# Performance work log

Hardware: AMD Instinct MI355X
Metric: run time of the kernel (lower is better)

## Reference

```python
import jax, jax.numpy as jnp
import numpy as np

N_SAMPLE = 32
RADIUS = 0.25
NORMALIZE_DP = True

B, N, K, C = 8, 8192, 2048, 64


def setup_inputs() -> dict:
    key = jax.random.key(0)
    k1, k2, k3 = jax.random.split(key, 3)
    points = jax.random.uniform(k1, (B, N, 3), dtype=jnp.float32)
    centroids = jax.random.uniform(k2, (B, K, 3), dtype=jnp.float32)
    features = jax.random.normal(k3, (B, C, N), dtype=jnp.float32)
    return {"points": points, "centroids": centroids, "features": features}


def _ball_query(points, centroids, n_sample, radius):
    # points: (B,N,3), centroids: (B,K,3) -> indices (B,K,n_sample) int32
    # squared distances via |c|^2 + |p|^2 - 2 c.p to avoid a (B,K,N,3) temp
    cp = jnp.einsum("bkd,bnd->bkn", centroids, points)  # (B,K,N)
    d2 = (
        jnp.sum(centroids * centroids, -1)[:, :, None]
        + jnp.sum(points * points, -1)[:, None, :]
        - 2.0 * cp
    )
    mask = d2 < radius * radius  # (B,K,N)
    # stable argsort on ~mask puts in-ball indices first, in ascending order
    order = jnp.argsort(jnp.logical_not(mask), axis=-1, stable=True)
    idx = order[..., :n_sample]  # (B,K,S)
    count = jnp.sum(mask, axis=-1, keepdims=True)  # (B,K,1)
    slot = jnp.arange(n_sample)[None, None, :]
    # CUDA ball_query semantics: pad empty slots with the first found index
    idx = jnp.where(slot < count, idx, idx[..., :1])
    return idx


def reference(points, centroids, features):
    idx = _ball_query(points, centroids, N_SAMPLE, RADIUS)  # (B,K,S)
    # gather points: (B,K,S,3)
    gp = jax.vmap(lambda p, i: p[i])(points, idx)
    gp = gp - centroids[:, :, None, :]  # centroid subtract
    if NORMALIZE_DP:
        gp = gp / RADIUS
    grouped_pts = jnp.transpose(gp, (0, 3, 1, 2))  # (B,3,K,S)
    # gather features: (B,C,K,S)
    new_feats = jax.vmap(lambda f, i: f[:, i])(features, idx)
    return grouped_pts, new_feats
```

## Files before the change

### kernel.cpp

```cpp
#include <hip/hip_runtime.h>

constexpr int B = 8;
constexpr int N = 8192;
constexpr int K = 2048;
constexpr int C = 64;
constexpr int NS = 32;
#define RAD2 0.0625f

__global__ __launch_bounds__(256) void ballquery_gp_kernel(
    const float* __restrict__ points,
    const float* __restrict__ centroids,
    float* __restrict__ gp_out,
    int* __restrict__ idx_ws)
{
#pragma clang fp contract(off)
    const int wave = (blockIdx.x * blockDim.x + threadIdx.x) >> 6;
    const int lane = threadIdx.x & 63;
    if (wave >= B * K) return;
    const int b = wave / K;
    const int k = wave - b * K;

    const float* cptr = centroids + (size_t)(b * K + k) * 3;
    const float c0 = cptr[0], c1 = cptr[1], c2 = cptr[2];
    const float cc = (c0 * c0 + c1 * c1) + c2 * c2;

    const float* pbase = points + (size_t)b * N * 3;
    int* idxrow = idx_ws + (size_t)wave * NS;
    float* gpb = gp_out + ((size_t)b * 3 * K + k) * NS;

    int count = 0;
    int idx0 = 0;

    for (int base = 0; base < N; base += 64) {
        const int i = base + lane;
        const float p0 = pbase[i * 3 + 0];
        const float p1 = pbase[i * 3 + 1];
        const float p2 = pbase[i * 3 + 2];
        const float pp = (p0 * p0 + p1 * p1) + p2 * p2;
        const float cp = (c0 * p0 + c1 * p1) + c2 * p2;
        const float d2 = (cc + pp) - 2.0f * cp;
        const bool hit = d2 < RAD2;
        const unsigned long long m = __ballot(hit);
        if (hit) {
            const unsigned long long below = m & ((1ull << lane) - 1ull);
            const int pos = count + __popcll(below);
            if (pos < NS) {
                idxrow[pos] = i;
                gpb[0 * K * NS + pos] = (p0 - c0) * 4.0f;
                gpb[1 * K * NS + pos] = (p1 - c1) * 4.0f;
                gpb[2 * K * NS + pos] = (p2 - c2) * 4.0f;
            }
        }
        if (count == 0 && m != 0ull) idx0 = base + __builtin_ctzll(m);
        count += __popcll(m);
        if (count >= NS) break;
    }

    const int cnt = count < NS ? count : NS;
    if (lane >= cnt && lane < NS) {
        const float p0 = pbase[idx0 * 3 + 0];
        const float p1 = pbase[idx0 * 3 + 1];
        const float p2 = pbase[idx0 * 3 + 2];
        idxrow[lane] = idx0;
        gpb[0 * K * NS + lane] = (p0 - c0) * 4.0f;
        gpb[1 * K * NS + lane] = (p1 - c1) * 4.0f;
        gpb[2 * K * NS + lane] = (p2 - c2) * 4.0f;
    }
}

__global__ __launch_bounds__(1024) void gather_feats_lds(
    const float* __restrict__ features,
    const int* __restrict__ idx_ws,
    float* __restrict__ nf_out)
{
    __shared__ float row[N];
    const int bc = blockIdx.x;
    const int t = threadIdx.x;

    {
        const float4* frow4 = reinterpret_cast<const float4*>(features + (size_t)bc * N);
        float4* row4 = reinterpret_cast<float4*>(row);
#pragma unroll
        for (int j = 0; j < 2; ++j)
            row4[t + j * 1024] = frow4[t + j * 1024];
    }
    __syncthreads();

    const int b = bc >> 6;
    const int* idxb = idx_ws + (size_t)b * K * NS;
    float* outb = nf_out + (size_t)bc * K * NS;

#pragma unroll
    for (int j = 0; j < 16; ++j) {
        const int g = j * 1024 + t;
        const int4 iv = *reinterpret_cast<const int4*>(idxb + (size_t)g * 4);
        float4 v;
        v.x = row[iv.x];
        v.y = row[iv.y];
        v.z = row[iv.z];
        v.w = row[iv.w];
        *reinterpret_cast<float4*>(outb + (size_t)g * 4) = v;
    }
}

extern "C" void kernel_launch(void* const* d_in, const int* in_sizes, int n_in,
                              void* d_out, int out_size, void* d_ws, size_t ws_size,
                              hipStream_t stream) {
    const float* points    = (const float*)d_in[0];
    const float* centroids = (const float*)d_in[1];
    const float* features  = (const float*)d_in[2];
    float* out = (float*)d_out;

    float* gp_out = out;
    float* nf_out = out + (size_t)B * 3 * K * NS;
    int* idx_ws = (int*)d_ws;

    const int waves = B * K;
    const int blocksA = waves / 4;
    hipLaunchKernelGGL(ballquery_gp_kernel, dim3(blocksA), dim3(256), 0, stream,
                       points, centroids, gp_out, idx_ws);

    hipLaunchKernelGGL(gather_feats_lds, dim3(B * C), dim3(1024), 0, stream,
                       features, idx_ws, nf_out);
}
```

Before: 61.06 us.

## Prefetch next point chunk, use nontemporal gather I/O, shrink ball-query blocks

In the ball-query kernel, the next 64-point chunk is software-prefetched into registers while the current chunk is tested, so load latency is hidden behind the distance computation. The block size drops from 256 to 128 threads and the div/mod is replaced with shifts. In the feature gather, index loads are double-buffered, and the feature-row loads and output stores use nontemporal builtins to reduce cache pollution. The prefetch adds one redundant chunk load per wave on early exit, and the nontemporal hints may interact unpredictably with L2 reuse.

```diff
diff --git a/kernel.cpp b/kernel.cpp
--- a/kernel.cpp
+++ b/kernel.cpp
@@ -7,7 +7,10 @@
 constexpr int NS = 32;
 #define RAD2 0.0625f
 
-__global__ __launch_bounds__(256) void ballquery_gp_kernel(
+typedef float  fx4 __attribute__((ext_vector_type(4)));
+typedef int    ix4 __attribute__((ext_vector_type(4)));
+
+__global__ __launch_bounds__(128) void ballquery_gp_kernel(
     const float* __restrict__ points,
     const float* __restrict__ centroids,
     float* __restrict__ gp_out,
@@ -17,8 +20,8 @@
     const int wave = (blockIdx.x * blockDim.x + threadIdx.x) >> 6;
     const int lane = threadIdx.x & 63;
     if (wave >= B * K) return;
-    const int b = wave / K;
-    const int k = wave - b * K;
+    const int b = wave >> 11;
+    const int k = wave & (K - 1);
 
     const float* cptr = centroids + (size_t)(b * K + k) * 3;
     const float c0 = cptr[0], c1 = cptr[1], c2 = cptr[2];
@@ -28,32 +31,40 @@
     int* idxrow = idx_ws + (size_t)wave * NS;
     float* gpb = gp_out + ((size_t)b * 3 * K + k) * NS;
 
+    const unsigned long long below_mask = (lane == 63) ? ~0ull >> 1
+                                                       : (1ull << lane) - 1ull;
+
     int count = 0;
     int idx0 = 0;
 
+    float q0 = pbase[lane * 3 + 0];
+    float q1 = pbase[lane * 3 + 1];
+    float q2 = pbase[lane * 3 + 2];
+
     for (int base = 0; base < N; base += 64) {
-        const int i = base + lane;
-        const float p0 = pbase[i * 3 + 0];
-        const float p1 = pbase[i * 3 + 1];
-        const float p2 = pbase[i * 3 + 2];
-        const float pp = (p0 * p0 + p1 * p1) + p2 * p2;
-        const float cp = (c0 * p0 + c1 * p1) + c2 * p2;
+        const int nb = (base + 64 < N) ? (base + 64 + lane) : lane;
+        const float n0 = pbase[nb * 3 + 0];
+        const float n1 = pbase[nb * 3 + 1];
+        const float n2 = pbase[nb * 3 + 2];
+
+        const float pp = (q0 * q0 + q1 * q1) + q2 * q2;
+        const float cp = (c0 * q0 + c1 * q1) + c2 * q2;
         const float d2 = (cc + pp) - 2.0f * cp;
         const bool hit = d2 < RAD2;
         const unsigned long long m = __ballot(hit);
         if (hit) {
-            const unsigned long long below = m & ((1ull << lane) - 1ull);
-            const int pos = count + __popcll(below);
+            const int pos = count + __popcll(m & below_mask);
             if (pos < NS) {
-                idxrow[pos] = i;
-                gpb[0 * K * NS + pos] = (p0 - c0) * 4.0f;
-                gpb[1 * K * NS + pos] = (p1 - c1) * 4.0f;
-                gpb[2 * K * NS + pos] = (p2 - c2) * 4.0f;
+                idxrow[pos] = base + lane;
+                gpb[0 * K * NS + pos] = (q0 - c0) * 4.0f;
+                gpb[1 * K * NS + pos] = (q1 - c1) * 4.0f;
+                gpb[2 * K * NS + pos] = (q2 - c2) * 4.0f;
             }
         }
         if (count == 0 && m != 0ull) idx0 = base + __builtin_ctzll(m);
         count += __popcll(m);
         if (count >= NS) break;
+        q0 = n0; q1 = n1; q2 = n2;
     }
 
     const int cnt = count < NS ? count : NS;
@@ -78,11 +89,11 @@
     const int t = threadIdx.x;
 
     {
-        const float4* frow4 = reinterpret_cast<const float4*>(features + (size_t)bc * N);
-        float4* row4 = reinterpret_cast<float4*>(row);
+        const fx4* frow4 = reinterpret_cast<const fx4*>(features + (size_t)bc * N);
+        fx4* row4 = reinterpret_cast<fx4*>(row);
 #pragma unroll
         for (int j = 0; j < 2; ++j)
-            row4[t + j * 1024] = frow4[t + j * 1024];
+            row4[t + j * 1024] = __builtin_nontemporal_load(&frow4[t + j * 1024]);
     }
     __syncthreads();
 
@@ -90,16 +101,20 @@
     const int* idxb = idx_ws + (size_t)b * K * NS;
     float* outb = nf_out + (size_t)bc * K * NS;
 
+    ix4 iv = *reinterpret_cast<const ix4*>(idxb + (size_t)t * 4);
 #pragma unroll
     for (int j = 0; j < 16; ++j) {
         const int g = j * 1024 + t;
-        const int4 iv = *reinterpret_cast<const int4*>(idxb + (size_t)g * 4);
-        float4 v;
+        ix4 ivn;
+        if (j < 15)
+            ivn = *reinterpret_cast<const ix4*>(idxb + (size_t)(g + 1024) * 4);
+        fx4 v;
         v.x = row[iv.x];
         v.y = row[iv.y];
         v.z = row[iv.z];
         v.w = row[iv.w];
-        *reinterpret_cast<float4*>(outb + (size_t)g * 4) = v;
+        __builtin_nontemporal_store(v, reinterpret_cast<fx4*>(outb + (size_t)g * 4));
+        if (j < 15) iv = ivn;
     }
 }
 
@@ -116,8 +131,7 @@
     int* idx_ws = (int*)d_ws;
 
     const int waves = B * K;
-    const int blocksA = waves / 4;
-    hipLaunchKernelGGL(ballquery_gp_kernel, dim3(blocksA), dim3(256), 0, stream,
+    hipLaunchKernelGGL(ballquery_gp_kernel, dim3(waves / 2), dim3(128), 0, stream,
                        points, centroids, gp_out, idx_ws);
 
     hipLaunchKernelGGL(gather_feats_lds, dim3(B * C), dim3(1024), 0, stream,
```

After: 56.80 us. 1.07x faster.
